# Kernel tuning notes

Measured on AMD Instinct MI355X. Metric: run time of the kernel, lower is better.

## Reference

```python
import jax, jax.numpy as jnp
import numpy as np

HID = 4096; NH = 32; NKV = 8; HD = 128; INTER = 14336
B = 4; S = 1024; T = B * S
LIMIT = 20.0; EPS = 1e-5; SCALE = HD ** -0.5; ROPE_BASE = 1e6


def _ln(x, w, b):
    m = jnp.mean(x, -1, keepdims=True)
    v = jnp.var(x, -1, keepdims=True)
    return (x - m) * jax.lax.rsqrt(v + EPS) * w + b


def _rope(x, cos, sin):
    # x: [T, nh, HD]; cos/sin: [T, HD//2]; neox-style half rotation
    d = HD // 2
    x1, x2 = x[..., :d], x[..., d:]
    c, s = cos[:, None, :], sin[:, None, :]
    return jnp.concatenate([x1 * c - x2 * s, x2 * c + x1 * s], axis=-1)


def _gegelu(x):
    a = jnp.minimum(x[..., ::2], LIMIT)              # gelu branch, clamp max only
    lin = jnp.clip(x[..., 1::2], -LIMIT, LIMIT)       # linear branch, clamp both
    return a * jax.nn.sigmoid(1.702 * a) * (lin + 1.0)


def setup_inputs():
    key = jax.random.key(0)
    ks = jax.random.split(key, 8)
    inv = 1.0 / (ROPE_BASE ** (np.arange(0, HD, 2, dtype=np.float64) / HD))
    pos = np.tile(np.arange(S), B)                    # positions per sequence
    freqs = pos[:, None] * inv[None, :]
    sd = 0.02
    return {
        "hidden_states": jax.random.normal(ks[0], (T, HID), jnp.float32) * sd,
        "residual": jax.random.normal(ks[1], (T, HID), jnp.float32) * sd,
        "cos": jnp.asarray(np.cos(freqs), jnp.float32),
        "sin": jnp.asarray(np.sin(freqs), jnp.float32),
        "cu_seqlen_prefill": jnp.arange(B + 1, dtype=jnp.int32) * S,
        "w_qkv": jax.random.normal(ks[2], (HID, (NH + 2 * NKV) * HD), jnp.float32) * sd,
        "b_qkv": jnp.zeros(((NH + 2 * NKV) * HD,), jnp.float32),
        "w_o": jax.random.normal(ks[3], (NH * HD, HID), jnp.float32) * sd,
        "w_ln1": jnp.ones((HID,), jnp.float32),
        "b_ln1": jnp.zeros((HID,), jnp.float32),
        "w_ln2": jnp.ones((HID,), jnp.float32),
        "b_ln2": jnp.zeros((HID,), jnp.float32),
        "w_up": jax.random.normal(ks[4], (HID, 2 * INTER), jnp.float32) * sd,
        "b_up": jnp.zeros((2 * INTER,), jnp.float32),
        "w_down": jax.random.normal(ks[5], (INTER, HID), jnp.float32) * sd,
        "b_down": jnp.zeros((HID,), jnp.float32),
    }


def reference(hidden_states, residual, cos, sin, cu_seqlen_prefill, w_qkv, b_qkv, w_o,
              w_ln1, b_ln1, w_ln2, b_ln2, w_up, b_up, w_down, b_down):
    # FastLayerNorm fused residual-add + LN
    h = hidden_states + residual
    normed = _ln(h, w_ln1, b_ln1)

    qkv = normed @ w_qkv + b_qkv
    q = qkv[:, :NH * HD].reshape(T, NH, HD)
    kv = qkv[:, NH * HD:].reshape(T, 2, NKV, HD)
    k, v = kv[:, 0], kv[:, 1]
    q = _rope(q, cos, sin)
    k = _rope(k, cos, sin)

    # prefill flash attention: equal-length sequences, causal, GQA
    qb = q.reshape(B, S, NH, HD)
    rep = NH // NKV
    kb = jnp.repeat(k.reshape(B, S, NKV, HD), rep, axis=2)
    vb = jnp.repeat(v.reshape(B, S, NKV, HD), rep, axis=2)
    scores = jnp.einsum('bqhd,bkhd->bhqk', qb, kb) * SCALE
    causal = jnp.tril(jnp.ones((S, S), bool))
    scores = jnp.where(causal[None, None], scores, jnp.finfo(scores.dtype).min)
    probs = jax.nn.softmax(scores, axis=-1)
    ctx = jnp.einsum('bhqk,bkhd->bqhd', probs, vb).reshape(T, NH * HD)

    attn_out = ctx @ w_o  # o_proj, bias=False

    h2 = attn_out + h
    normed2 = _ln(h2, w_ln2, b_ln2)
    mlp_out = _gegelu(normed2 @ w_up + b_up) @ w_down + b_down
    return (mlp_out, h2)
```

## Files before the change

kernel.cpp:

```cpp
#include <hip/hip_runtime.h>
#include <stdint.h>
#include <stddef.h>

#define TT     4096
#define HIDN   4096
#define NHEAD  32
#define NKVH   8
#define HDIM   128
#define INTERN 14336
#define QKVN   6144
#define SEQL   1024

typedef unsigned short u16;
typedef __attribute__((ext_vector_type(4))) float f32x4;
typedef __attribute__((ext_vector_type(8))) short s16x8;
typedef __attribute__((ext_vector_type(4))) unsigned short u16x4;

__device__ __forceinline__ u16 f2bf(float f) {
  union { float f; unsigned u; } un; un.f = f;
  unsigned r = un.u + 0x7fffu + ((un.u >> 16) & 1u);
  return (u16)(r >> 16);
}
__device__ __forceinline__ float bf2f(u16 h) {
  union { unsigned u; float f; } un; un.u = ((unsigned)h) << 16;
  return un.f;
}
__device__ __forceinline__ void gl_lds16(const void* g, void* l) {
  __builtin_amdgcn_global_load_lds((const __attribute__((address_space(1))) void*)g,
                                   (__attribute__((address_space(3))) void*)l, 16, 0, 0);
}

__global__ __launch_bounds__(256) void add_ln_kernel(
    const float* __restrict__ x, const float* __restrict__ res,
    const float* __restrict__ w, const float* __restrict__ b,
    float* __restrict__ h_out, u16* __restrict__ normed)
{
  const int row = blockIdx.x;
  const int tid = threadIdx.x;
  const size_t base = (size_t)row * HIDN;
  float4 v[4];
  float sum = 0.f, sq = 0.f;
#pragma unroll
  for (int i = 0; i < 4; ++i) {
    const int idx = (tid + i * 256) * 4;
    float4 a = *(const float4*)(x + base + idx);
    if (res) {
      float4 r2 = *(const float4*)(res + base + idx);
      a.x += r2.x; a.y += r2.y; a.z += r2.z; a.w += r2.w;
    }
    v[i] = a;
    sum += a.x + a.y + a.z + a.w;
    sq  += a.x * a.x + a.y * a.y + a.z * a.z + a.w * a.w;
  }
  __shared__ float red[8];
  const int lane = tid & 63, wv = tid >> 6;
#pragma unroll
  for (int off = 32; off >= 1; off >>= 1) {
    sum += __shfl_down(sum, off);
    sq  += __shfl_down(sq, off);
  }
  if (lane == 0) { red[wv] = sum; red[4 + wv] = sq; }
  __syncthreads();
  sum = red[0] + red[1] + red[2] + red[3];
  sq  = red[4] + red[5] + red[6] + red[7];
  const float mean = sum * (1.f / HIDN);
  const float var  = sq * (1.f / HIDN) - mean * mean;
  const float rstd = rsqrtf(var + 1e-5f);
#pragma unroll
  for (int i = 0; i < 4; ++i) {
    const int idx = (tid + i * 256) * 4;
    if (h_out) *(float4*)(h_out + base + idx) = v[i];
    float4 wv4 = *(const float4*)(w + idx);
    float4 bv4 = *(const float4*)(b + idx);
    u16x4 o;
    o.x = f2bf((v[i].x - mean) * rstd * wv4.x + bv4.x);
    o.y = f2bf((v[i].y - mean) * rstd * wv4.y + bv4.y);
    o.z = f2bf((v[i].z - mean) * rstd * wv4.z + bv4.z);
    o.w = f2bf((v[i].w - mean) * rstd * wv4.w + bv4.w);
    *(u16x4*)(normed + base + idx) = o;
  }
}

__global__ __launch_bounds__(256) void convtrans_kernel(
    const float* __restrict__ W, u16* __restrict__ Wt, const int K, const int N)
{
  __shared__ float tile[64 * 65];
  const int k0 = blockIdx.x * 64;
  const int n0 = blockIdx.y * 64;
  const int tid = threadIdx.x;
  const int c4 = (tid & 15) * 4;
  const int r  = tid >> 4;
#pragma unroll
  for (int p = 0; p < 4; ++p) {
    const int rr = r + p * 16;
    float4 v4 = *(const float4*)(W + (size_t)(k0 + rr) * N + n0 + c4);
    tile[rr * 65 + c4 + 0] = v4.x;
    tile[rr * 65 + c4 + 1] = v4.y;
    tile[rr * 65 + c4 + 2] = v4.z;
    tile[rr * 65 + c4 + 3] = v4.w;
  }
  __syncthreads();
#pragma unroll
  for (int p = 0; p < 4; ++p) {
    const int nl = r + p * 16;
    u16x4 o;
    o.x = f2bf(tile[(c4 + 0) * 65 + nl]);
    o.y = f2bf(tile[(c4 + 1) * 65 + nl]);
    o.z = f2bf(tile[(c4 + 2) * 65 + nl]);
    o.w = f2bf(tile[(c4 + 3) * 65 + nl]);
    *(u16x4*)(Wt + (size_t)(n0 + nl) * K + k0 + c4) = o;
  }
}

template <int MODE>
__global__ __launch_bounds__(256) void gemm_bt_kernel(
    const u16* __restrict__ A, const u16* __restrict__ Bt,
    const float* __restrict__ bias, const float* __restrict__ addsrc,
    void* __restrict__ Cout, const int N, const int K, const int ldc)
{
  __shared__ u16 As[128 * 32];
  __shared__ u16 Bs[128 * 32];

  const int grid_n = N >> 7;
  const int pid = blockIdx.x;
  const int npg = 8 * grid_n;
  const int bm = (pid / npg) * 8 + (pid & 7);
  const int bn = (pid % npg) >> 3;

  const int tid  = threadIdx.x;
  const int lane = tid & 63;
  const int wv   = tid >> 6;
  const int wm = wv >> 1, wn = wv & 1;
  const int quad = lane >> 4, l16 = lane & 15;

  const int srow = tid >> 2;
  const int scol = (tid & 3) * 8;
  const u16* Ag = A  + (size_t)(bm * 128 + srow) * K + scol;
  const u16* Bg = Bt + (size_t)(bn * 128 + srow) * K + scol;
  u16* AsW = As + wv * 512;
  u16* BsW = Bs + wv * 512;

  const u16* Apos = As + (wm * 64 + l16) * 32 + quad * 8;
  const u16* Bpos = Bs + (wn * 64 + l16) * 32 + quad * 8;

  f32x4 acc[4][4] = {};

  for (int k0 = 0; k0 < K; k0 += 32) {
    __syncthreads();
    gl_lds16(Ag + k0, AsW);
    gl_lds16(Ag + (size_t)64 * K + k0, AsW + 2048);
    gl_lds16(Bg + k0, BsW);
    gl_lds16(Bg + (size_t)64 * K + k0, BsW + 2048);
    __syncthreads();
    s16x8 af[4], bfr[4];
#pragma unroll
    for (int i = 0; i < 4; ++i) af[i]  = *(const s16x8*)(Apos + i * 512);
#pragma unroll
    for (int j = 0; j < 4; ++j) bfr[j] = *(const s16x8*)(Bpos + j * 512);
#pragma unroll
    for (int i = 0; i < 4; ++i)
#pragma unroll
      for (int j = 0; j < 4; ++j)
        acc[i][j] = __builtin_amdgcn_mfma_f32_16x16x32_bf16(af[i], bfr[j], acc[i][j], 0, 0, 0);
  }

#pragma unroll
  for (int i = 0; i < 4; ++i) {
    const int row0 = bm * 128 + wm * 64 + i * 16 + quad * 4;
#pragma unroll
    for (int j = 0; j < 4; ++j) {
      const int col = bn * 128 + wn * 64 + j * 16 + l16;
#pragma unroll
      for (int rr = 0; rr < 4; ++rr) {
        float vv = acc[i][j][rr];
        if (MODE == 0) {
          ((u16*)Cout)[(size_t)(row0 + rr) * ldc + col] = f2bf(vv + bias[col]);
        } else if (MODE == 1) {
          const size_t off = (size_t)(row0 + rr) * ldc + col;
          ((float*)Cout)[off] = vv + addsrc[off];
        } else if (MODE == 2) {
          ((float*)Cout)[(size_t)(row0 + rr) * ldc + col] = vv + bias[col];
        } else {
          vv += bias[col];
          float other = __shfl_xor(vv, 1);
          if ((l16 & 1) == 0) {
            float aa  = fminf(vv, 20.f);
            float lin = fminf(fmaxf(other, -20.f), 20.f);
            float g = aa / (1.f + __expf(-1.702f * aa)) * (lin + 1.f);
            ((u16*)Cout)[(size_t)(row0 + rr) * ldc + (col >> 1)] = f2bf(g);
          }
        }
      }
    }
  }
}

__global__ __launch_bounds__(256) void rope_kernel(
    u16* __restrict__ qkv, const float* __restrict__ cosb, const float* __restrict__ sinb)
{
  const int idx  = blockIdx.x * 256 + threadIdx.x;
  const int d    = idx & 63;
  const int rest = idx >> 6;
  const int hh   = rest % 40;
  const int t    = rest / 40;
  const int col  = (hh < 32) ? hh * 128 : 4096 + (hh - 32) * 128;
  const size_t base = (size_t)t * QKVN + col;
  const float x1 = bf2f(qkv[base + d]);
  const float x2 = bf2f(qkv[base + d + 64]);
  const float c = cosb[t * 64 + d];
  const float s = sinb[t * 64 + d];
  qkv[base + d]      = f2bf(x1 * c - x2 * s);
  qkv[base + d + 64] = f2bf(x2 * c + x1 * s);
}

__global__ __launch_bounds__(256) void flash_kernel(
    const u16* __restrict__ qkv, u16* __restrict__ ctx)
{
  __shared__ u16 Qs[64 * 128];
  __shared__ u16 Ks[64 * 128];
  __shared__ u16 Vt[128 * 72];
  __shared__ u16 Ps[4 * 16 * 72];

  const int qt = (int)gridDim.x - 1 - (int)blockIdx.x;
  const int h  = blockIdx.y;
  const int bz = blockIdx.z;
  const int kvh = h >> 2;

  const int tid = threadIdx.x, lane = tid & 63, wv = tid >> 6;
  const int quad = lane >> 4, l16 = lane & 15;

  const size_t tok0 = (size_t)bz * SEQL + (size_t)qt * 64;
  const u16* qg  = qkv + tok0 * QKVN + h * HDIM;
  const u16* kg0 = qkv + (size_t)bz * SEQL * QKVN + 4096 + kvh * HDIM;
  const u16* vg0 = qkv + (size_t)bz * SEQL * QKVN + 5120 + kvh * HDIM;

  const int qrow = tid >> 4;
  const int qcol = (tid & 15) * 8;
#pragma unroll
  for (int j = 0; j < 4; ++j)
    gl_lds16(qg + (size_t)(j * 16 + qrow) * QKVN + qcol, Qs + j * 2048 + wv * 512);

  f32x4 oacc[8] = {};
  float m_i[4], l_i[4];
#pragma unroll
  for (int r = 0; r < 4; ++r) { m_i[r] = -INFINITY; l_i[r] = 0.f; }

  const int vhd = tid & 127;
  const int vkq = tid >> 7;

  for (int kt = 0; kt <= qt; ++kt) {
    __syncthreads();
    const u16* kg = kg0 + (size_t)(kt * 64) * QKVN;
    const u16* vg = vg0 + (size_t)(kt * 64) * QKVN;
#pragma unroll
    for (int j = 0; j < 4; ++j)
      gl_lds16(kg + (size_t)(j * 16 + qrow) * QKVN + qcol, Ks + j * 2048 + wv * 512);
#pragma unroll
    for (int j = 0; j < 8; ++j) {
      const int kk0 = (j * 2 + vkq) * 4;
      u16x4 pk;
      pk.x = vg[(size_t)(kk0 + 0) * QKVN + vhd];
      pk.y = vg[(size_t)(kk0 + 1) * QKVN + vhd];
      pk.z = vg[(size_t)(kk0 + 2) * QKVN + vhd];
      pk.w = vg[(size_t)(kk0 + 3) * QKVN + vhd];
      *(u16x4*)(Vt + vhd * 72 + kk0) = pk;
    }
    __syncthreads();

    f32x4 sacc[4] = {};
#pragma unroll
    for (int ks = 0; ks < 4; ++ks) {
      s16x8 aq = *(const s16x8*)(Qs + (wv * 16 + l16) * 128 + ks * 32 + quad * 8);
#pragma unroll
      for (int jt = 0; jt < 4; ++jt) {
        s16x8 bk = *(const s16x8*)(Ks + (jt * 16 + l16) * 128 + ks * 32 + quad * 8);
        sacc[jt] = __builtin_amdgcn_mfma_f32_16x16x32_bf16(aq, bk, sacc[jt], 0, 0, 0);
      }
    }

    const bool diag = (kt == qt);
    const int qrb = wv * 16 + quad * 4;
#pragma unroll
    for (int jt = 0; jt < 4; ++jt)
#pragma unroll
      for (int r = 0; r < 4; ++r) {
        float sv = sacc[jt][r] * 0.08838834764831845f;
        if (diag && (jt * 16 + l16) > (qrb + r)) sv = -INFINITY;
        sacc[jt][r] = sv;
      }

    float alpha[4];
#pragma unroll
    for (int r = 0; r < 4; ++r) {
      float mx = fmaxf(fmaxf(sacc[0][r], sacc[1][r]), fmaxf(sacc[2][r], sacc[3][r]));
      mx = fmaxf(mx, __shfl_xor(mx, 1));
      mx = fmaxf(mx, __shfl_xor(mx, 2));
      mx = fmaxf(mx, __shfl_xor(mx, 4));
      mx = fmaxf(mx, __shfl_xor(mx, 8));
      const float mn = fmaxf(m_i[r], mx);
      alpha[r] = __expf(m_i[r] - mn);
      m_i[r] = mn;
    }
#pragma unroll
    for (int jt = 0; jt < 4; ++jt)
#pragma unroll
      for (int r = 0; r < 4; ++r)
        sacc[jt][r] = __expf(sacc[jt][r] - m_i[r]);
#pragma unroll
    for (int r = 0; r < 4; ++r) {
      float sm = sacc[0][r] + sacc[1][r] + sacc[2][r] + sacc[3][r];
      sm += __shfl_xor(sm, 1);
      sm += __shfl_xor(sm, 2);
      sm += __shfl_xor(sm, 4);
      sm += __shfl_xor(sm, 8);
      l_i[r] = l_i[r] * alpha[r] + sm;
    }
#pragma unroll
    for (int t8 = 0; t8 < 8; ++t8)
#pragma unroll
      for (int r = 0; r < 4; ++r)
        oacc[t8][r] *= alpha[r];

    u16* Pw = Ps + wv * 1152;
#pragma unroll
    for (int jt = 0; jt < 4; ++jt)
#pragma unroll
      for (int r = 0; r < 4; ++r)
        Pw[(quad * 4 + r) * 72 + jt * 16 + l16] = f2bf(sacc[jt][r]);

#pragma unroll
    for (int ks2 = 0; ks2 < 2; ++ks2) {
      s16x8 ap = *(const s16x8*)(Pw + l16 * 72 + ks2 * 32 + quad * 8);
#pragma unroll
      for (int t8 = 0; t8 < 8; ++t8) {
        s16x8 bv = *(const s16x8*)(Vt + (t8 * 16 + l16) * 72 + ks2 * 32 + quad * 8);
        oacc[t8] = __builtin_amdgcn_mfma_f32_16x16x32_bf16(ap, bv, oacc[t8], 0, 0, 0);
      }
    }
  }

  float inv[4];
#pragma unroll
  for (int r = 0; r < 4; ++r) inv[r] = 1.f / l_i[r];
#pragma unroll
  for (int t8 = 0; t8 < 8; ++t8)
#pragma unroll
    for (int r = 0; r < 4; ++r) {
      const size_t row = tok0 + wv * 16 + quad * 4 + r;
      ctx[row * (size_t)HIDN + h * HDIM + t8 * 16 + l16] = f2bf(oacc[t8][r] * inv[r]);
    }
}

extern "C" void kernel_launch(void* const* d_in, const int* in_sizes, int n_in,
                              void* d_out, int out_size, void* d_ws, size_t ws_size,
                              hipStream_t stream) {
  (void)in_sizes; (void)n_in; (void)out_size; (void)ws_size;
  const float* hs    = (const float*)d_in[0];
  const float* resid = (const float*)d_in[1];
  const float* cosb  = (const float*)d_in[2];
  const float* sinb  = (const float*)d_in[3];
  const float* w_qkv = (const float*)d_in[5];
  const float* b_qkv = (const float*)d_in[6];
  const float* w_o   = (const float*)d_in[7];
  const float* w_ln1 = (const float*)d_in[8];
  const float* b_ln1 = (const float*)d_in[9];
  const float* w_ln2 = (const float*)d_in[10];
  const float* b_ln2 = (const float*)d_in[11];
  const float* w_up  = (const float*)d_in[12];
  const float* b_up  = (const float*)d_in[13];
  const float* w_dn  = (const float*)d_in[14];
  const float* b_dn  = (const float*)d_in[15];

  float* mlp_out = (float*)d_out;
  float* h2      = mlp_out + (size_t)TT * HIDN;

  char* ws = (char*)d_ws;
  float* h_buf  = (float*)ws;
  u16*   normed = (u16*)(ws + 67108864ULL);
  u16*   qkv    = (u16*)(ws + 100663296ULL);
  u16*   ctx    = (u16*)(ws + 150994944ULL);
  u16*   act    = (u16*)(ws + 100663296ULL);
  u16*   warena = (u16*)(ws + 218103808ULL);

  add_ln_kernel<<<TT, 256, 0, stream>>>(hs, resid, w_ln1, b_ln1, h_buf, normed);
  convtrans_kernel<<<dim3(HIDN / 64, QKVN / 64), 256, 0, stream>>>(w_qkv, warena, HIDN, QKVN);
  gemm_bt_kernel<0><<<(TT / 128) * (QKVN / 128), 256, 0, stream>>>(
      normed, warena, b_qkv, nullptr, qkv, QKVN, HIDN, QKVN);
  rope_kernel<<<(TT * 40 * 64) / 256, 256, 0, stream>>>(qkv, cosb, sinb);
  flash_kernel<<<dim3(SEQL / 64, NHEAD, 4), 256, 0, stream>>>(qkv, ctx);
  convtrans_kernel<<<dim3(HIDN / 64, HIDN / 64), 256, 0, stream>>>(w_o, warena, HIDN, HIDN);
  gemm_bt_kernel<1><<<(TT / 128) * (HIDN / 128), 256, 0, stream>>>(
      ctx, warena, nullptr, h_buf, h2, HIDN, HIDN, HIDN);
  add_ln_kernel<<<TT, 256, 0, stream>>>(h2, nullptr, w_ln2, b_ln2, nullptr, normed);
  convtrans_kernel<<<dim3(HIDN / 64, (2 * INTERN) / 64), 256, 0, stream>>>(w_up, warena, HIDN, 2 * INTERN);
  gemm_bt_kernel<3><<<(TT / 128) * ((2 * INTERN) / 128), 256, 0, stream>>>(
      normed, warena, b_up, nullptr, act, 2 * INTERN, HIDN, INTERN);
  convtrans_kernel<<<dim3(INTERN / 64, HIDN / 64), 256, 0, stream>>>(w_dn, warena, INTERN, HIDN);
  gemm_bt_kernel<2><<<(TT / 128) * (HIDN / 128), 256, 0, stream>>>(
      act, warena, b_dn, nullptr, mlp_out, HIDN, INTERN, HIDN);
}
```

Measured before the change: 4.003 ms.

## Replace 128x128 GEMM with 256x256 double-buffered, swizzled, pipelined 8-wave kernel

The bf16 GEMM moves from 128x128x32 tiles with 4 waves and a single LDS buffer to 256x256x64 tiles with 8 waves. Global-to-LDS loads are double-buffered and issued while the MFMAs run, with explicit vmcnt waits, barriers and setprio. An XOR swizzle on the LDS columns avoids bank conflicts, and the tile-to-block mapping is remapped with an XCD-aware scheme. The aim is higher MFMA utilisation and data reuse on the dominant GEMMs. The cost is heavy LDS use (128KB per block) and fragile hand-written wait counts.

```diff
diff --git a/kernel.cpp b/kernel.cpp
--- a/kernel.cpp
+++ b/kernel.cpp
@@ -113,63 +113,112 @@
 }
 
 template <int MODE>
-__global__ __launch_bounds__(256) void gemm_bt_kernel(
+__global__ __launch_bounds__(512, 2) void gemm256_kernel(
     const u16* __restrict__ A, const u16* __restrict__ Bt,
     const float* __restrict__ bias, const float* __restrict__ addsrc,
     void* __restrict__ Cout, const int N, const int K, const int ldc)
 {
-  __shared__ u16 As[128 * 32];
-  __shared__ u16 Bs[128 * 32];
-
-  const int grid_n = N >> 7;
-  const int pid = blockIdx.x;
-  const int npg = 8 * grid_n;
-  const int bm = (pid / npg) * 8 + (pid & 7);
-  const int bn = (pid % npg) >> 3;
+  __shared__ u16 As[2][256 * 64];
+  __shared__ u16 Bs[2][256 * 64];
+
+  const int NT = K >> 6;
+  const int grid_n = N >> 8;
+  const int nwg = (int)gridDim.x;
+  const int cpx = nwg >> 3;
+  const int pid = (int)blockIdx.x;
+  const int vid = (pid & 7) * cpx + (pid >> 3);
+  const int bm = vid / grid_n;
+  const int bn = vid % grid_n;
 
   const int tid  = threadIdx.x;
   const int lane = tid & 63;
   const int wv   = tid >> 6;
-  const int wm = wv >> 1, wn = wv & 1;
+  const int wm   = wv >> 2;
+  const int wn   = wv & 3;
   const int quad = lane >> 4, l16 = lane & 15;
 
-  const int srow = tid >> 2;
-  const int scol = (tid & 3) * 8;
-  const u16* Ag = A  + (size_t)(bm * 128 + srow) * K + scol;
-  const u16* Bg = Bt + (size_t)(bn * 128 + srow) * K + scol;
-  u16* AsW = As + wv * 512;
-  u16* BsW = Bs + wv * 512;
-
-  const u16* Apos = As + (wm * 64 + l16) * 32 + quad * 8;
-  const u16* Bpos = Bs + (wn * 64 + l16) * 32 + quad * 8;
-
-  f32x4 acc[4][4] = {};
-
-  for (int k0 = 0; k0 < K; k0 += 32) {
-    __syncthreads();
-    gl_lds16(Ag + k0, AsW);
-    gl_lds16(Ag + (size_t)64 * K + k0, AsW + 2048);
-    gl_lds16(Bg + k0, BsW);
-    gl_lds16(Bg + (size_t)64 * K + k0, BsW + 2048);
-    __syncthreads();
-    s16x8 af[4], bfr[4];
-#pragma unroll
-    for (int i = 0; i < 4; ++i) af[i]  = *(const s16x8*)(Apos + i * 512);
-#pragma unroll
-    for (int j = 0; j < 4; ++j) bfr[j] = *(const s16x8*)(Bpos + j * 512);
-#pragma unroll
-    for (int i = 0; i < 4; ++i)
-#pragma unroll
-      for (int j = 0; j < 4; ++j)
-        acc[i][j] = __builtin_amdgcn_mfma_f32_16x16x32_bf16(af[i], bfr[j], acc[i][j], 0, 0, 0);
-  }
-
-#pragma unroll
-  for (int i = 0; i < 4; ++i) {
-    const int row0 = bm * 128 + wm * 64 + i * 16 + quad * 4;
+  const int stRow = tid >> 3;
+  const int csrc  = ((tid & 7) ^ (stRow & 7)) * 8;
+  const u16* Abase = A  + ((size_t)bm * 256 + stRow) * K + csrc;
+  const u16* Bbase = Bt + ((size_t)bn * 256 + stRow) * K + csrc;
+
+  auto stg = [&](int kt, bool isA, int L) {
+    const int kts = (kt < NT) ? kt : 0;
+    const u16* g = (isA ? Abase : Bbase) + (size_t)L * 64 * K + (size_t)kts * 64;
+    u16* d = (isA ? As[kt & 1] : Bs[kt & 1]) + (L * 64 + wv * 8) * 64;
+    gl_lds16(g, d);
+  };
+
+  const int cswz0 = (((0 * 4 + quad)) ^ (l16 & 7)) * 16;
+  const int cswz1 = (((1 * 4 + quad)) ^ (l16 & 7)) * 16;
+  const int arow  = (wm * 128 + l16) * 128;
+  const int brow  = (wn * 64 + l16) * 128;
+
+  stg(0, false, 0); stg(0, false, 1); stg(0, false, 2); stg(0, false, 3);
+  stg(0, true, 0);  stg(0, true, 2);  stg(0, true, 1);  stg(0, true, 3);
+  stg(1, false, 0); stg(1, false, 1); stg(1, false, 2); stg(1, false, 3);
+  stg(1, true, 0);  stg(1, true, 2);
+  asm volatile("s_waitcnt vmcnt(6)" ::: "memory");
+  __builtin_amdgcn_s_barrier();
+  asm volatile("" ::: "memory");
+
+  f32x4 acc[8][4] = {};
+
+  for (int t = 0; t < NT; ++t) {
+    const int cur = t & 1;
+    const char* Ab = (const char*)As[cur];
+    const char* Bb = (const char*)Bs[cur];
+    s16x8 bfr[4][2];
+#pragma unroll
+    for (int p = 0; p < 4; ++p) {
+      s16x8 af[2][2];
+#pragma unroll
+      for (int i = 0; i < 2; ++i) {
+        af[i][0] = *(const s16x8*)(Ab + arow + (p * 2 + i) * 2048 + cswz0);
+        af[i][1] = *(const s16x8*)(Ab + arow + (p * 2 + i) * 2048 + cswz1);
+      }
+      if (p == 0) {
+#pragma unroll
+        for (int j = 0; j < 4; ++j) {
+          bfr[j][0] = *(const s16x8*)(Bb + brow + j * 2048 + cswz0);
+          bfr[j][1] = *(const s16x8*)(Bb + brow + j * 2048 + cswz1);
+        }
+        stg(t + 1, true, 1); stg(t + 1, true, 3);
+      } else if (p == 1) {
+        stg(t + 2, false, 0); stg(t + 2, false, 1);
+      } else if (p == 2) {
+        stg(t + 2, false, 2); stg(t + 2, false, 3);
+      } else {
+        stg(t + 2, true, 0); stg(t + 2, true, 2);
+        asm volatile("s_waitcnt vmcnt(6)" ::: "memory");
+      }
+      asm volatile("" ::: "memory");
+      __builtin_amdgcn_s_barrier();
+      asm volatile("" ::: "memory");
+      __builtin_amdgcn_s_setprio(1);
+#pragma unroll
+      for (int i = 0; i < 2; ++i)
+#pragma unroll
+        for (int j = 0; j < 4; ++j) {
+          acc[p * 2 + i][j] = __builtin_amdgcn_mfma_f32_16x16x32_bf16(
+              af[i][0], bfr[j][0], acc[p * 2 + i][j], 0, 0, 0);
+          acc[p * 2 + i][j] = __builtin_amdgcn_mfma_f32_16x16x32_bf16(
+              af[i][1], bfr[j][1], acc[p * 2 + i][j], 0, 0, 0);
+        }
+      __builtin_amdgcn_s_setprio(0);
+      asm volatile("" ::: "memory");
+      __builtin_amdgcn_s_barrier();
+      asm volatile("" ::: "memory");
+    }
+  }
+  asm volatile("s_waitcnt vmcnt(0)" ::: "memory");
+
+#pragma unroll
+  for (int i = 0; i < 8; ++i) {
+    const int row0 = bm * 256 + wm * 128 + i * 16 + quad * 4;
 #pragma unroll
     for (int j = 0; j < 4; ++j) {
-      const int col = bn * 128 + wn * 64 + j * 16 + l16;
+      const int col = bn * 256 + wn * 64 + j * 16 + l16;
 #pragma unroll
       for (int rr = 0; rr < 4; ++rr) {
         float vv = acc[i][j][rr];
@@ -384,18 +433,18 @@
 
   add_ln_kernel<<<TT, 256, 0, stream>>>(hs, resid, w_ln1, b_ln1, h_buf, normed);
   convtrans_kernel<<<dim3(HIDN / 64, QKVN / 64), 256, 0, stream>>>(w_qkv, warena, HIDN, QKVN);
-  gemm_bt_kernel<0><<<(TT / 128) * (QKVN / 128), 256, 0, stream>>>(
+  gemm256_kernel<0><<<(TT / 256) * (QKVN / 256), 512, 0, stream>>>(
       normed, warena, b_qkv, nullptr, qkv, QKVN, HIDN, QKVN);
   rope_kernel<<<(TT * 40 * 64) / 256, 256, 0, stream>>>(qkv, cosb, sinb);
   flash_kernel<<<dim3(SEQL / 64, NHEAD, 4), 256, 0, stream>>>(qkv, ctx);
   convtrans_kernel<<<dim3(HIDN / 64, HIDN / 64), 256, 0, stream>>>(w_o, warena, HIDN, HIDN);
-  gemm_bt_kernel<1><<<(TT / 128) * (HIDN / 128), 256, 0, stream>>>(
+  gemm256_kernel<1><<<(TT / 256) * (HIDN / 256), 512, 0, stream>>>(
       ctx, warena, nullptr, h_buf, h2, HIDN, HIDN, HIDN);
   add_ln_kernel<<<TT, 256, 0, stream>>>(h2, nullptr, w_ln2, b_ln2, nullptr, normed);
   convtrans_kernel<<<dim3(HIDN / 64, (2 * INTERN) / 64), 256, 0, stream>>>(w_up, warena, HIDN, 2 * INTERN);
-  gemm_bt_kernel<3><<<(TT / 128) * ((2 * INTERN) / 128), 256, 0, stream>>>(
+  gemm256_kernel<3><<<(TT / 256) * ((2 * INTERN) / 256), 512, 0, stream>>>(
       normed, warena, b_up, nullptr, act, 2 * INTERN, HIDN, INTERN);
   convtrans_kernel<<<dim3(INTERN / 64, HIDN / 64), 256, 0, stream>>>(w_dn, warena, INTERN, HIDN);
-  gemm_bt_kernel<2><<<(TT / 128) * (HIDN / 128), 256, 0, stream>>>(
+  gemm256_kernel<2><<<(TT / 256) * (HIDN / 256), 512, 0, stream>>>(
       act, warena, b_dn, nullptr, mlp_out, HIDN, INTERN, HIDN);
 }
```

After: 3.364 ms. -16.0%, faster.
